# Performance work log

Measured on AMD Instinct MI355X. Metric: run time of the kernel, lower is better.

Reference implementation:

```python
import jax, jax.numpy as jnp
import numpy as np

EPS = 1e-12  # matches torch F.normalize default eps
SCALE = 64.0  # fixed softmax temperature from the source

def _l2_normalize(x, axis):
    n = jnp.linalg.norm(x, ord=2, axis=axis, keepdims=True)
    return x / jnp.maximum(n, EPS)

def setup_inputs() -> dict:
    key = jax.random.key(0)
    k1, k2, k3 = jax.random.split(key, 3)
    B, L, S, D = 8, 2048, 2048, 128
    return {
        "query": jax.random.normal(k1, (B, L, D), dtype=jnp.float32),
        "key": jax.random.normal(k2, (B, S, D), dtype=jnp.float32),
        "value": jax.random.normal(k3, (B, S, D), dtype=jnp.float32),
    }

def reference(query, key, value):
    # rank-3 query path with norm=True, return_value=True, return_score=False
    q = _l2_normalize(query, axis=2)   # [B, L, D]
    k = _l2_normalize(key, axis=2)     # [B, S, D]
    score = jnp.einsum('nlk,nsk->nls', q, k)            # [B, L, S]
    score = jax.nn.softmax(score * SCALE, axis=2)
    # original does broadcast-multiply-then-sum; equivalent contraction:
    out = jnp.einsum('nls,nsd->nld', score, value)      # [B, L, D]
    return out
```

## Files before the change

kernel.cpp:

```cpp
#include <hip/hip_runtime.h>
#include <stdint.h>

#define Bb 8
#define Ll 2048
#define Ss 2048
#define Dd 128
#define NSB 4
#define SCHUNK 512
#define NROWS 16384
#define SCALE_LOG2E 92.33248261689366f

typedef __attribute__((ext_vector_type(8))) short bf16x8;
typedef __attribute__((ext_vector_type(4))) float f32x4;
typedef __attribute__((ext_vector_type(16))) float f32x16;
typedef __attribute__((ext_vector_type(4))) unsigned u32x4;

__device__ __forceinline__ unsigned f2bf_pack(float a, float b) {
  unsigned ua = __float_as_uint(a); ua += 0x7fffu + ((ua >> 16) & 1u);
  unsigned ub = __float_as_uint(b); ub += 0x7fffu + ((ub >> 16) & 1u);
  return (ua >> 16) | (ub & 0xffff0000u);
}

__device__ __forceinline__ void gl_lds16(const void* g, void* l) {
  __builtin_amdgcn_global_load_lds(
      (const __attribute__((address_space(1))) unsigned*)g,
      (__attribute__((address_space(3))) unsigned*)l, 16, 0, 0);
}

#define TRS 138
extern "C" __global__ __launch_bounds__(256)
void prep_kern(const float* __restrict__ Q, const float* __restrict__ K,
               const float* __restrict__ V,
               unsigned short* __restrict__ Qn, unsigned short* __restrict__ Kn,
               unsigned short* __restrict__ Vt) {
  __shared__ unsigned short T[32 * TRS];
  const int t = threadIdx.x;
  const int bid = blockIdx.x;
  if (bid < 8192) {
    const int lane = t & 63;
    int row = (bid << 2) + (t >> 6);
    int r = row;
    const float* src = Q; unsigned short* dst = Qn;
    if (row >= NROWS) { r = row - NROWS; src = K; dst = Kn; }
    float2 f = *(const float2*)(src + (size_t)r * Dd + lane * 2);
    float ss = f.x * f.x + f.y * f.y;
#pragma unroll
    for (int m = 1; m < 64; m <<= 1) ss += __shfl_xor(ss, m, 64);
    float inv = 1.0f / fmaxf(sqrtf(ss), 1e-12f);
    *(unsigned*)(dst + (size_t)r * Dd + lane * 2) = f2bf_pack(f.x * inv, f.y * inv);
  } else {
    const int vb = bid - 8192;
    const int b = vb & 7, sw = vb >> 3;
    const int d4 = t & 31, sr = t >> 5;
#pragma unroll
    for (int p = 0; p < 4; ++p) {
      int sl = p * 8 + sr;
      float4 v = *(const float4*)(V + ((size_t)(b * Ss + sw * 32 + sl)) * Dd + d4 * 4);
      *(unsigned*)&T[sl * TRS + d4 * 4]     = f2bf_pack(v.x, v.y);
      *(unsigned*)&T[sl * TRS + d4 * 4 + 2] = f2bf_pack(v.z, v.w);
    }
    __syncthreads();
    const int so = t & 3, db = t >> 2;
#pragma unroll
    for (int p = 0; p < 2; ++p) {
      int d = p * 64 + db;
      unsigned u[4];
#pragma unroll
      for (int k = 0; k < 4; ++k) {
        unsigned lo = T[(so * 8 + 2 * k) * TRS + d];
        unsigned hi = T[(so * 8 + 2 * k + 1) * TRS + d];
        u[k] = lo | (hi << 16);
      }
      *(uint4*)(Vt + ((size_t)(b * Dd + d)) * Ss + sw * 32 + so * 8) =
          make_uint4(u[0], u[1], u[2], u[3]);
    }
  }
}

extern "C" __global__ __launch_bounds__(256, 2)
void attn_kern(const unsigned short* __restrict__ Qn,
               const unsigned short* __restrict__ Kn,
               const unsigned short* __restrict__ Vt,
               unsigned short* __restrict__ Op,
               float* __restrict__ Mp, float* __restrict__ Lp) {
  __shared__ unsigned short Kl[2][16 * 512];
  __shared__ unsigned short Vl[2][16 * 512];
  const int tid = threadIdx.x, wv = tid >> 6, lane = tid & 63;
  const int lm = lane & 31, h = lane >> 5;
  const int gid = blockIdx.x;
  const int grp = gid & 31, qt = gid >> 5;
  const int b = grp >> 2, sb = grp & 3;
  const int sbase = sb * SCHUNK;
  const int qrow = qt * 128 + wv * 32 + lm;

  const unsigned short* Qrow = Qn + ((size_t)(b * Ll + qrow)) * Dd;
  bf16x8 qf[8];
#pragma unroll
  for (int kt = 0; kt < 8; ++kt)
    qf[kt] = *(const bf16x8*)(Qrow + kt * 16 + h * 8);

  const unsigned short* Kb = Kn + (size_t)b * Ss * Dd;
  const unsigned short* Vb = Vt + (size_t)b * Dd * Ss;

  f32x16 o[4];
#pragma unroll
  for (int i = 0; i < 4; ++i)
#pragma unroll
    for (int r = 0; r < 16; ++r) o[i][r] = 0.f;

  auto stage = [&](int it, int buf) {
    const int s0 = sbase + it * 64;
#pragma unroll
    for (int i = 0; i < 4; ++i) {
      const int ks = wv * 4 + i;
      gl_lds16(Kb + (size_t)(s0 + (ks >> 3) * 32 + lm) * Dd + (ks & 7) * 16 + h * 8,
               &Kl[buf][ks * 512]);
    }
#pragma unroll
    for (int i = 0; i < 4; ++i) {
      const int vs = wv * 4 + i;
      gl_lds16(Vb + (size_t)((vs >> 2) * 32 + lm) * Ss + s0 + (vs & 3) * 16 + h * 8,
               &Vl[buf][vs * 512]);
    }
  };
  stage(0, 0);

  float mrun = -1e30f, lrun = 0.f;

#pragma unroll 1
  for (int it = 0; it < 8; ++it) {
    __syncthreads();
    const int cur = it & 1;
    if (it + 1 < 8) stage(it + 1, cur ^ 1);

    f32x16 st[2];
#pragma unroll
    for (int sblk = 0; sblk < 2; ++sblk) {
      f32x16 acc;
#pragma unroll
      for (int r = 0; r < 16; ++r) acc[r] = 0.f;
#pragma unroll
      for (int kt = 0; kt < 8; ++kt) {
        bf16x8 kf = *(const bf16x8*)&Kl[cur][(sblk * 8 + kt) * 512 + lane * 8];
        acc = __builtin_amdgcn_mfma_f32_32x32x16_bf16(kf, qf[kt], acc, 0, 0, 0);
      }
      st[sblk] = acc;
    }

    float vmax = st[0][0];
#pragma unroll
    for (int r = 0; r < 16; ++r) vmax = fmaxf(vmax, fmaxf(st[0][r], st[1][r]));
    vmax = fmaxf(vmax, __shfl_xor(vmax, 32, 64));
    const float mnew = fmaxf(mrun, vmax * SCALE_LOG2E);
    const float alpha = __builtin_amdgcn_exp2f(mrun - mnew);
    mrun = mnew;
#pragma unroll
    for (int i = 0; i < 4; ++i)
#pragma unroll
      for (int r = 0; r < 16; ++r) o[i][r] *= alpha;

    float ls = 0.f;
#pragma unroll
    for (int t = 0; t < 4; ++t) {
      float p[8];
#pragma unroll
      for (int j = 0; j < 8; ++j) {
        p[j] = __builtin_amdgcn_exp2f(st[t >> 1][(t & 1) * 8 + j] * SCALE_LOG2E - mnew);
        ls += p[j];
      }
      unsigned u0 = f2bf_pack(p[0], p[1]), u1 = f2bf_pack(p[2], p[3]);
      unsigned u2 = f2bf_pack(p[4], p[5]), u3 = f2bf_pack(p[6], p[7]);
      unsigned s0 = (unsigned)__shfl_xor((int)u0, 32, 64);
      unsigned s1 = (unsigned)__shfl_xor((int)u1, 32, 64);
      unsigned s2 = (unsigned)__shfl_xor((int)u2, 32, 64);
      unsigned s3 = (unsigned)__shfl_xor((int)u3, 32, 64);
      u32x4 fr;
      fr.x = h ? s2 : u0;
      fr.y = h ? s3 : u1;
      fr.z = h ? u2 : s0;
      fr.w = h ? u3 : s1;
      bf16x8 pf = __builtin_bit_cast(bf16x8, fr);
#pragma unroll
      for (int dblk = 0; dblk < 4; ++dblk) {
        bf16x8 vf = *(const bf16x8*)&Vl[cur][(dblk * 4 + t) * 512 + lane * 8];
        o[dblk] = __builtin_amdgcn_mfma_f32_32x32x16_bf16(vf, pf, o[dblk], 0, 0, 0);
      }
    }
    lrun = lrun * alpha + ls;
  }

  const float lt = lrun + __shfl_xor(lrun, 32, 64);
  unsigned short* Ob = Op + ((size_t)sb * NROWS + b * Ll + qrow) * Dd;
#pragma unroll
  for (int dblk = 0; dblk < 4; ++dblk)
#pragma unroll
    for (int g = 0; g < 4; ++g) {
      uint2 w;
      w.x = f2bf_pack(o[dblk][g * 4 + 0], o[dblk][g * 4 + 1]);
      w.y = f2bf_pack(o[dblk][g * 4 + 2], o[dblk][g * 4 + 3]);
      *(uint2*)(Ob + dblk * 32 + g * 8 + h * 4) = w;
    }
  if (h == 0) {
    Mp[sb * NROWS + b * Ll + qrow] = mrun;
    Lp[sb * NROWS + b * Ll + qrow] = lt;
  }
}

extern "C" __global__ __launch_bounds__(256)
void comb_kern(const unsigned short* __restrict__ Op, const float* __restrict__ Mp,
               const float* __restrict__ Lp, float* __restrict__ Out) {
  const int idx = blockIdx.x * 256 + threadIdx.x;
  const int row = idx >> 5;
  const int dof = (idx & 31) * 4;
  float m[NSB], w[NSB];
  float M = -1e30f;
#pragma unroll
  for (int s = 0; s < NSB; ++s) { m[s] = Mp[s * NROWS + row]; M = fmaxf(M, m[s]); }
  float den = 0.f;
#pragma unroll
  for (int s = 0; s < NSB; ++s) {
    w[s] = __builtin_amdgcn_exp2f(m[s] - M);
    den += Lp[s * NROWS + row] * w[s];
  }
  float a0 = 0.f, a1 = 0.f, a2 = 0.f, a3 = 0.f;
#pragma unroll
  for (int s = 0; s < NSB; ++s) {
    uint2 v = *(const uint2*)(Op + ((size_t)s * NROWS + row) * Dd + dof);
    a0 += w[s] * __uint_as_float(v.x << 16);
    a1 += w[s] * __uint_as_float(v.x & 0xffff0000u);
    a2 += w[s] * __uint_as_float(v.y << 16);
    a3 += w[s] * __uint_as_float(v.y & 0xffff0000u);
  }
  const float inv = 1.f / den;
  float4 r; r.x = a0 * inv; r.y = a1 * inv; r.z = a2 * inv; r.w = a3 * inv;
  *(float4*)(Out + (size_t)row * Dd + dof) = r;
}

extern "C" void kernel_launch(void* const* d_in, const int* in_sizes, int n_in,
                              void* d_out, int out_size, void* d_ws, size_t ws_size,
                              hipStream_t stream) {
  const float* Q = (const float*)d_in[0];
  const float* K = (const float*)d_in[1];
  const float* V = (const float*)d_in[2];
  float* Out = (float*)d_out;
  unsigned short* Qn = (unsigned short*)d_ws;
  unsigned short* Kn = Qn + (size_t)NROWS * Dd;
  unsigned short* Vt = Kn + (size_t)NROWS * Dd;
  unsigned short* Op = Vt + (size_t)Bb * Dd * Ss;
  float* Mp = (float*)(Op + (size_t)NSB * NROWS * Dd);
  float* Lp = Mp + (size_t)NSB * NROWS;
  hipLaunchKernelGGL(prep_kern, dim3(8192 + 512), dim3(256), 0, stream, Q, K, V, Qn, Kn, Vt);
  hipLaunchKernelGGL(attn_kern, dim3(512), dim3(256), 0, stream, Qn, Kn, Vt, Op, Mp, Lp);
  hipLaunchKernelGGL(comb_kern, dim3(2048), dim3(256), 0, stream, Op, Mp, Lp, Out);
}
```

Measured before the change: 113.6 us.

## Use fixed softmax max from unit-norm bound and hardware bf16 packing

Since normalized query and key make every score lie in [-1,1], the softmax shift is fixed at the scale constant instead of tracked online. This drops the per-tile max reduction, the rescaling of the output accumulators, and the max partials that the combine kernel read and exponentiated. It also swaps the manual bf16 rounding for the hardware packed-convert builtin when available. The trade-off is a risk of precision loss when scores are far below the bound, since tiny exponentials are stored in bf16.

```diff
diff --git a/kernel.cpp b/kernel.cpp
--- a/kernel.cpp
+++ b/kernel.cpp
@@ -11,7 +11,6 @@
 #define SCALE_LOG2E 92.33248261689366f
 
 typedef __attribute__((ext_vector_type(8))) short bf16x8;
-typedef __attribute__((ext_vector_type(4))) float f32x4;
 typedef __attribute__((ext_vector_type(16))) float f32x16;
 typedef __attribute__((ext_vector_type(4))) unsigned u32x4;
 
@@ -19,6 +18,15 @@
   unsigned ua = __float_as_uint(a); ua += 0x7fffu + ((ua >> 16) & 1u);
   unsigned ub = __float_as_uint(b); ub += 0x7fffu + ((ub >> 16) & 1u);
   return (ua >> 16) | (ub & 0xffff0000u);
+}
+
+__device__ __forceinline__ unsigned pkbf(float a, float b) {
+#if __has_builtin(__builtin_amdgcn_cvt_pk_bf16_f32)
+  auto r = __builtin_amdgcn_cvt_pk_bf16_f32(a, b);
+  return __builtin_bit_cast(unsigned, r);
+#else
+  return f2bf_pack(a, b);
+#endif
 }
 
 __device__ __forceinline__ void gl_lds16(const void* g, void* l) {
@@ -47,7 +55,7 @@
 #pragma unroll
     for (int m = 1; m < 64; m <<= 1) ss += __shfl_xor(ss, m, 64);
     float inv = 1.0f / fmaxf(sqrtf(ss), 1e-12f);
-    *(unsigned*)(dst + (size_t)r * Dd + lane * 2) = f2bf_pack(f.x * inv, f.y * inv);
+    *(unsigned*)(dst + (size_t)r * Dd + lane * 2) = pkbf(f.x * inv, f.y * inv);
   } else {
     const int vb = bid - 8192;
     const int b = vb & 7, sw = vb >> 3;
@@ -56,8 +64,8 @@
     for (int p = 0; p < 4; ++p) {
       int sl = p * 8 + sr;
       float4 v = *(const float4*)(V + ((size_t)(b * Ss + sw * 32 + sl)) * Dd + d4 * 4);
-      *(unsigned*)&T[sl * TRS + d4 * 4]     = f2bf_pack(v.x, v.y);
-      *(unsigned*)&T[sl * TRS + d4 * 4 + 2] = f2bf_pack(v.z, v.w);
+      *(unsigned*)&T[sl * TRS + d4 * 4]     = pkbf(v.x, v.y);
+      *(unsigned*)&T[sl * TRS + d4 * 4 + 2] = pkbf(v.z, v.w);
     }
     __syncthreads();
     const int so = t & 3, db = t >> 2;
@@ -82,7 +90,7 @@
                const unsigned short* __restrict__ Kn,
                const unsigned short* __restrict__ Vt,
                unsigned short* __restrict__ Op,
-               float* __restrict__ Mp, float* __restrict__ Lp) {
+               float* __restrict__ Lp) {
   __shared__ unsigned short Kl[2][16 * 512];
   __shared__ unsigned short Vl[2][16 * 512];
   const int tid = threadIdx.x, wv = tid >> 6, lane = tid & 63;
@@ -125,7 +133,7 @@
   };
   stage(0, 0);
 
-  float mrun = -1e30f, lrun = 0.f;
+  float lrun = 0.f;
 
 #pragma unroll 1
   for (int it = 0; it < 8; ++it) {
@@ -147,29 +155,17 @@
       st[sblk] = acc;
     }
 
-    float vmax = st[0][0];
-#pragma unroll
-    for (int r = 0; r < 16; ++r) vmax = fmaxf(vmax, fmaxf(st[0][r], st[1][r]));
-    vmax = fmaxf(vmax, __shfl_xor(vmax, 32, 64));
-    const float mnew = fmaxf(mrun, vmax * SCALE_LOG2E);
-    const float alpha = __builtin_amdgcn_exp2f(mrun - mnew);
-    mrun = mnew;
-#pragma unroll
-    for (int i = 0; i < 4; ++i)
-#pragma unroll
-      for (int r = 0; r < 16; ++r) o[i][r] *= alpha;
-
     float ls = 0.f;
 #pragma unroll
     for (int t = 0; t < 4; ++t) {
       float p[8];
 #pragma unroll
-      for (int j = 0; j < 8; ++j) {
-        p[j] = __builtin_amdgcn_exp2f(st[t >> 1][(t & 1) * 8 + j] * SCALE_LOG2E - mnew);
-        ls += p[j];
-      }
-      unsigned u0 = f2bf_pack(p[0], p[1]), u1 = f2bf_pack(p[2], p[3]);
-      unsigned u2 = f2bf_pack(p[4], p[5]), u3 = f2bf_pack(p[6], p[7]);
+      for (int j = 0; j < 8; ++j)
+        p[j] = __builtin_amdgcn_exp2f(
+            __builtin_fmaf(st[t >> 1][(t & 1) * 8 + j], SCALE_LOG2E, -SCALE_LOG2E));
+      ls += ((p[0] + p[1]) + (p[2] + p[3])) + ((p[4] + p[5]) + (p[6] + p[7]));
+      unsigned u0 = pkbf(p[0], p[1]), u1 = pkbf(p[2], p[3]);
+      unsigned u2 = pkbf(p[4], p[5]), u3 = pkbf(p[6], p[7]);
       unsigned s0 = (unsigned)__shfl_xor((int)u0, 32, 64);
       unsigned s1 = (unsigned)__shfl_xor((int)u1, 32, 64);
       unsigned s2 = (unsigned)__shfl_xor((int)u2, 32, 64);
@@ -186,7 +182,7 @@
         o[dblk] = __builtin_amdgcn_mfma_f32_32x32x16_bf16(vf, pf, o[dblk], 0, 0, 0);
       }
     }
-    lrun = lrun * alpha + ls;
+    lrun += ls;
   }
 
   const float lt = lrun + __shfl_xor(lrun, 32, 64);
@@ -196,40 +192,30 @@
 #pragma unroll
     for (int g = 0; g < 4; ++g) {
       uint2 w;
-      w.x = f2bf_pack(o[dblk][g * 4 + 0], o[dblk][g * 4 + 1]);
-      w.y = f2bf_pack(o[dblk][g * 4 + 2], o[dblk][g * 4 + 3]);
+      w.x = pkbf(o[dblk][g * 4 + 0], o[dblk][g * 4 + 1]);
+      w.y = pkbf(o[dblk][g * 4 + 2], o[dblk][g * 4 + 3]);
       *(uint2*)(Ob + dblk * 32 + g * 8 + h * 4) = w;
     }
-  if (h == 0) {
-    Mp[sb * NROWS + b * Ll + qrow] = mrun;
-    Lp[sb * NROWS + b * Ll + qrow] = lt;
-  }
+  if (h == 0) Lp[sb * NROWS + b * Ll + qrow] = lt;
 }
 
 extern "C" __global__ __launch_bounds__(256)
-void comb_kern(const unsigned short* __restrict__ Op, const float* __restrict__ Mp,
+void comb_kern(const unsigned short* __restrict__ Op,
                const float* __restrict__ Lp, float* __restrict__ Out) {
   const int idx = blockIdx.x * 256 + threadIdx.x;
   const int row = idx >> 5;
   const int dof = (idx & 31) * 4;
-  float m[NSB], w[NSB];
-  float M = -1e30f;
-#pragma unroll
-  for (int s = 0; s < NSB; ++s) { m[s] = Mp[s * NROWS + row]; M = fmaxf(M, m[s]); }
   float den = 0.f;
 #pragma unroll
-  for (int s = 0; s < NSB; ++s) {
-    w[s] = __builtin_amdgcn_exp2f(m[s] - M);
-    den += Lp[s * NROWS + row] * w[s];
-  }
+  for (int s = 0; s < NSB; ++s) den += Lp[s * NROWS + row];
   float a0 = 0.f, a1 = 0.f, a2 = 0.f, a3 = 0.f;
 #pragma unroll
   for (int s = 0; s < NSB; ++s) {
     uint2 v = *(const uint2*)(Op + ((size_t)s * NROWS + row) * Dd + dof);
-    a0 += w[s] * __uint_as_float(v.x << 16);
-    a1 += w[s] * __uint_as_float(v.x & 0xffff0000u);
-    a2 += w[s] * __uint_as_float(v.y << 16);
-    a3 += w[s] * __uint_as_float(v.y & 0xffff0000u);
+    a0 += __uint_as_float(v.x << 16);
+    a1 += __uint_as_float(v.x & 0xffff0000u);
+    a2 += __uint_as_float(v.y << 16);
+    a3 += __uint_as_float(v.y & 0xffff0000u);
   }
   const float inv = 1.f / den;
   float4 r; r.x = a0 * inv; r.y = a1 * inv; r.z = a2 * inv; r.w = a3 * inv;
@@ -247,9 +233,8 @@
   unsigned short* Kn = Qn + (size_t)NROWS * Dd;
   unsigned short* Vt = Kn + (size_t)NROWS * Dd;
   unsigned short* Op = Vt + (size_t)Bb * Dd * Ss;
-  float* Mp = (float*)(Op + (size_t)NSB * NROWS * Dd);
-  float* Lp = Mp + (size_t)NSB * NROWS;
+  float* Lp = (float*)(Op + (size_t)NSB * NROWS * Dd);
   hipLaunchKernelGGL(prep_kern, dim3(8192 + 512), dim3(256), 0, stream, Q, K, V, Qn, Kn, Vt);
-  hipLaunchKernelGGL(attn_kern, dim3(512), dim3(256), 0, stream, Qn, Kn, Vt, Op, Mp, Lp);
-  hipLaunchKernelGGL(comb_kern, dim3(2048), dim3(256), 0, stream, Op, Mp, Lp, Out);
-}
+  hipLaunchKernelGGL(attn_kern, dim3(512), dim3(256), 0, stream, Qn, Kn, Vt, Op, Lp);
+  hipLaunchKernelGGL(comb_kern, dim3(2048), dim3(256), 0, stream, Op, Lp, Out);
+}
```

Measured after the change: 110.8 us. 2.5% less time.
